# Performance work log

Hardware: AMD Instinct MI355X
Metric: run time of the kernel (lower is better)

## Reference

```python
import jax, jax.numpy as jnp
import numpy as np

B, C, D, H, W = 2, 2, 64, 256, 256
EPS = 1e-6
ALPHA = 5.0
TTEMP = 0.7


def _grids():
    gy, gx = jnp.meshgrid(jnp.arange(H, dtype=jnp.float32),
                          jnp.arange(W, dtype=jnp.float32), indexing='ij')
    return gy, gx


def _extract_targets(centerlines, gy, gx):
    # centerlines: [B,1,D,H,W] int labels {0,1,2}. For each (b,d) slice: if label i
    # occurs exactly once, target = (y,x) of that pixel, else negpair (-1,-1).
    cl = centerlines[:, 0]  # [B,D,H,W]
    out = []
    for lbl in (1, 2):
        m = (cl == lbl).astype(jnp.float32)
        cnt = m.sum(axis=(-2, -1))            # [B,D]
        ys = (m * gy).sum(axis=(-2, -1))
        xs = (m * gx).sum(axis=(-2, -1))
        t = jnp.where((cnt == 1.0)[..., None], jnp.stack([ys, xs], axis=-1), -1.0)
        out.append(t)                          # [B,D,2] float32
    return out


def _d2(gy, gx, target):
    # torch PairwiseDistance adds eps to the difference: ||x1-x2+eps||_2
    # -> [B,1,D,H,W]
    dy = gy[None, None, None] - target[:, None, :, 0, None, None] + EPS
    dx = gx[None, None, None] - target[:, None, :, 1, None, None] + EPS
    return jnp.sqrt(dy * dy + dx * dx)


def total_loss(logits, centerlines, radiuses):
    probs = jax.nn.sigmoid(logits)             # [B,2,D,H,W]
    gy, gx = _grids()
    targets = _extract_targets(centerlines, gy, gx)
    d2s = [_d2(gy, gx, t) for t in targets]
    # art masks: relu(exp(d2/r1 - 1) - 1) then filled with 1 where >0  ==  (d2 > r1);
    # the in-place fill makes it gradient-free, so treat as constant {0,1} mask.
    arts = [jax.lax.stop_gradient((d2s[k] > radiuses[k, 1]).astype(jnp.float32))
            for k in range(2)]
    arts = [arts[1], arts[0]]                  # swapped, exactly as in the source
    valid = [(t[:, :, 0] != -1.0).astype(jnp.float32) for t in targets]  # [B,D]

    # ---- CenterDistanceLoss ----
    loss_cent = jnp.float32(0.0)
    for k in range(2):
        art = arts[k]                                            # [B,1,D,H,W]
        denom = (probs * art).sum(axis=(1, 3, 4)) + EPS          # [B,D]
        y_cnt = (art * gy * probs).sum(axis=(1, 3, 4)) / denom
        x_cnt = (art * gx * probs).sum(axis=(1, 3, 4)) / denom
        cnt = jnp.stack([y_cnt, x_cnt], axis=-1)                 # [B,D,2]
        diff = cnt - targets[k] + EPS
        l2 = jnp.sqrt((diff * diff).sum(-1)) * valid[k]
        loss_cent = loss_cent + l2.mean()

    # ---- RadiusConstraintLoss ----
    loss_cnst = jnp.float32(0.0)
    for k in range(2):
        r_lu, r_ow = radiuses[k, 0], radiuses[k, 1]
        vm = valid[k][:, None, :, None, None]                    # [B,1,D,1,1]
        d2 = d2s[k]
        art = arts[k]
        lu_dout = jax.nn.relu(1.0 - jnp.exp(1.0 - d2 / r_lu)) / ALPHA * vm * art
        ow_dout = jax.nn.relu(1.0 - jnp.exp(1.0 - d2 / r_ow)) / ALPHA * vm * art
        p_lu, p_ow = probs[:, :1], probs[:, 1:]
        rc_out = ((lu_dout * p_lu).sum(axis=(1, 3, 4)) / (p_lu.sum(axis=(1, 3, 4)) + EPS)
                  + (ow_dout * p_ow).sum(axis=(1, 3, 4)) / (p_ow.sum(axis=(1, 3, 4)) + EPS))
        lu_din = jax.nn.relu(jnp.exp(1.0 - d2 / r_lu) - 1.0) * vm
        ow_din = jax.nn.relu(jnp.exp(1.0 - d2 / r_ow) - 1.0) * vm
        rc_in = ((lu_din * (1.0 - p_lu)).sum(axis=(1, 3, 4)) / (r_lu * r_lu * jnp.pi)
                 + (ow_din * (1.0 - p_ow)).sum(axis=(1, 3, 4)) / (r_ow * r_ow * jnp.pi))
        loss_cnst = loss_cnst + rc_out.mean() + rc_in.mean()

    # ---- ConsistencyLoss ----  (F.softmax default dim=1 for 5-D; BCE clamps log >= -100)
    p_orig = jax.lax.stop_gradient(jax.nn.softmax(logits[:, :, 1:-1] / TTEMP, axis=1))
    p_shift = jax.nn.softmax(logits[:, :, 0:-2] / TTEMP, axis=1)
    log_p = jnp.maximum(jnp.log(p_orig), -100.0)
    log_1mp = jnp.maximum(jnp.log(1.0 - p_orig), -100.0)
    loss_csis = -(p_shift * log_p + (1.0 - p_shift) * log_1mp).mean()

    return 0.02 * loss_cent + 1.0 * loss_cnst + 0.001 * loss_csis


def setup_inputs():
    key = jax.random.key(0)
    k1, k2, k3, k4, k5 = jax.random.split(key, 5)
    logits = jax.random.normal(k1, (B, C, D, H, W), dtype=jnp.float32)
    # place exactly one ICA(=1) and one ECA(=2) marker per (b,d) slice
    ys1 = jax.random.randint(k2, (B * D,), 0, H)
    xs1 = jax.random.randint(k3, (B * D,), 0, W)
    ys2 = jax.random.randint(k4, (B * D,), 0, H)
    xs2 = jax.random.randint(k5, (B * D,), 0, W)
    bi = jnp.repeat(jnp.arange(B), D)
    di = jnp.tile(jnp.arange(D), B)
    cl = jnp.zeros((B, 1, D, H, W), dtype=jnp.int32)
    cl = cl.at[bi, 0, di, ys1, xs1].set(1)
    cl = cl.at[bi, 0, di, ys2, xs2].set(2)
    cl = cl.at[:, :, 0].set(0)  # exercise the negpair (-1,-1) path
    radiuses = jnp.array([[4.0, 7.0], [5.0, 8.0]], dtype=jnp.float32)
    return {"logits": logits, "centerlines": cl, "radiuses": radiuses}


def reference(logits, centerlines, radiuses):
    return total_loss(logits, centerlines, radiuses)
```

## Files before the change

### kernel.cpp

```cpp
#include <hip/hip_runtime.h>
#include <math.h>

#define BB 2
#define CC 2
#define DD 64
#define HW 65536
#define NROW 128
#define EPSF 1e-6f
#define ALPHAF 5.0f
#define BPR 8
#define LOG2E 1.44269504089f
#define LN2 0.69314718056f
#define INV_T (1.0f/0.7f)
#define C_SH (INV_T*LOG2E)

struct Ws {
  int   cnt[2][NROW];
  int   ysum[2][NROW];
  int   xsum[2][NROW];
  float tgt[2][NROW][2];
  float valid[2][NROW];
  float part[NROW][BPR][17];
};

__device__ __forceinline__ void scan4(const int4& v, long long i4,
                                      Ws* __restrict__ ws) {
  if ((v.x | v.y | v.z | v.w) == 0) return;
  int vv[4] = {v.x, v.y, v.z, v.w};
#pragma unroll
  for (int e = 0; e < 4; ++e) {
    int val = vv[e];
    if (val == 1 || val == 2) {
      long long idx = i4 * 4 + e;
      int hw  = (int)(idx & (HW - 1));
      int row = (int)(idx >> 16);
      int k = val - 1;
      atomicAdd(&ws->cnt[k][row], 1);
      atomicAdd(&ws->ysum[k][row], hw >> 8);
      atomicAdd(&ws->xsum[k][row], hw & 255);
    }
  }
}

__global__ __launch_bounds__(256) void k_extract(const int* __restrict__ cl,
                                                 Ws* __restrict__ ws) {
  const long long base = (long long)blockIdx.x * 1024 + threadIdx.x;
  const int4* p = (const int4*)cl;
  int4 a = p[base];
  int4 b = p[base + 256];
  int4 c = p[base + 512];
  int4 d = p[base + 768];
  scan4(a, base, ws);
  scan4(b, base + 256, ws);
  scan4(c, base + 512, ws);
  scan4(d, base + 768, ws);
}

struct RowCtx {
  float t0y, t0x, t1y, t1x;
  float r01sq, r11sq;
  float c00, c01, c10, c11;
};

template<bool N0, bool N1>
__device__ __forceinline__ void do_row(const float4& v0, const float4& v1,
                                       const float4& w0, const float4& w1,
                                       float yf, float x0f,
                                       const RowCtx& cx, float* acc)
{
  const float a0[4] = {v0.x, v0.y, v0.z, v0.w};
  const float a1[4] = {v1.x, v1.y, v1.z, v1.w};
  const float b0[4] = {w0.x, w0.y, w0.z, w0.w};
  const float b1[4] = {w1.x, w1.y, w1.z, w1.w};
  float rp0 = 0.f, rp1 = 0.f, rcs = 0.f, rpsx = 0.f;
  float rA0 = 0.f, rA0x = 0.f, rT00 = 0.f, rT01 = 0.f;
  float rA1 = 0.f, rA1x = 0.f, rT10 = 0.f, rT11 = 0.f;
  const float dy0 = yf - cx.t0y;
  const float dy0sq = dy0 * dy0;
  const float dy1 = yf - cx.t1y;
  const float dy1sq = dy1 * dy1;
#pragma unroll
  for (int e = 0; e < 4; ++e) {
    const float le0 = a0[e], le1 = a1[e];
    const float p0 = __builtin_amdgcn_rcpf(1.f + __expf(-le0));
    const float p1 = __builtin_amdgcn_rcpf(1.f + __expf(-le1));
    rp0 += p0; rp1 += p1;
    const float psum = p0 + p1;
    const float gxf = x0f + (float)e;

    const float dshn = (le1 - le0) * C_SH;
    const float psig = __builtin_amdgcn_rcpf(1.f + exp2f(dshn));
    const float dor2 = (b0[e] - b1[e]) * C_SH;
    const float lg  = log2f(1.f + exp2f(-fabsf(dor2)));
    const float sp2 = fmaxf(dor2, 0.f) + lg;
    rcs += psig * dor2 - sp2;

    float ap0 = p0, ap1 = p1, bp0 = p0, bp1 = p1;
    float d0sq = 0.f, d1sq = 0.f;
    if (N1) {
      const float dx1 = gxf - cx.t1x;
      d1sq = fmaf(dx1, dx1, dy1sq);
      const float art0 = (d1sq > cx.r11sq) ? 1.f : 0.f;
      ap0 = art0 * p0; ap1 = art0 * p1;
      const float a0p = ap0 + ap1;
      rA0 += a0p; rA0x = fmaf(gxf, a0p, rA0x);
      if (!N0) { rT00 += ap0; rT01 += ap1; }
    }
    if (N0) {
      const float dx0 = gxf - cx.t0x;
      d0sq = fmaf(dx0, dx0, dy0sq);
      const float art1 = (d0sq > cx.r01sq) ? 1.f : 0.f;
      bp0 = art1 * p0; bp1 = art1 * p1;
      const float a1p = bp0 + bp1;
      rA1 += a1p; rA1x = fmaf(gxf, a1p, rA1x);
      if (!N1) { rT10 += bp0; rT11 += bp1; }
    }
    if (!N0 || !N1) rpsx = fmaf(gxf, psum, rpsx);

    if (N0) {
      const float dist0 = __builtin_amdgcn_sqrtf(d0sq);
      const float elu0 = exp2f(fmaf(dist0, -cx.c00, LOG2E));
      const float eow0 = exp2f(fmaf(dist0, -cx.c01, LOG2E));
      acc[8]  = fmaf(fmaxf(1.f - elu0, 0.f), ap0, acc[8]);
      acc[9]  = fmaf(fmaxf(1.f - eow0, 0.f), ap1, acc[9]);
      acc[10] = fmaf(fmaxf(elu0 - 1.f, 0.f), 1.f - p0, acc[10]);
      acc[11] = fmaf(fmaxf(eow0 - 1.f, 0.f), 1.f - p1, acc[11]);
    }
    if (N1) {
      const float dist1 = __builtin_amdgcn_sqrtf(d1sq);
      const float elu1 = exp2f(fmaf(dist1, -cx.c10, LOG2E));
      const float eow1 = exp2f(fmaf(dist1, -cx.c11, LOG2E));
      acc[12] = fmaf(fmaxf(1.f - elu1, 0.f), bp0, acc[12]);
      acc[13] = fmaf(fmaxf(1.f - eow1, 0.f), bp1, acc[13]);
      acc[14] = fmaf(fmaxf(elu1 - 1.f, 0.f), 1.f - p0, acc[14]);
      acc[15] = fmaf(fmaxf(eow1 - 1.f, 0.f), 1.f - p1, acc[15]);
    }
  }
  acc[6] += rp0; acc[7] += rp1; acc[16] += rcs;
  const float rps = rp0 + rp1;
  if (N1) { acc[0] += rA0; acc[1] = fmaf(yf, rA0, acc[1]); acc[2] += rA0x; }
  else    { acc[0] += rps; acc[1] = fmaf(yf, rps, acc[1]); acc[2] += rpsx; }
  if (N0) { acc[3] += rA1; acc[4] = fmaf(yf, rA1, acc[4]); acc[5] += rA1x; }
  else    { acc[3] += rps; acc[4] = fmaf(yf, rps, acc[4]); acc[5] += rpsx; }
  if (!N0) { acc[8]  += N1 ? rT00 : rp0; acc[9]  += N1 ? rT01 : rp1; }
  if (!N1) { acc[12] += N0 ? rT10 : rp0; acc[13] += N0 ? rT11 : rp1; }
}

#define DISPATCH_ROW(V0,V1,W0,W1,YF)                                       \
  { const bool nr0 = fabsf((YF) - cx.t0y) <= cut0;                         \
    const bool nr1 = fabsf((YF) - cx.t1y) <= cut1;                         \
    if (nr0) { if (nr1) do_row<true ,true >(V0,V1,W0,W1,YF,x0f,cx,acc);    \
               else     do_row<true ,false>(V0,V1,W0,W1,YF,x0f,cx,acc); }  \
    else     { if (nr1) do_row<false,true >(V0,V1,W0,W1,YF,x0f,cx,acc);    \
               else     do_row<false,false>(V0,V1,W0,W1,YF,x0f,cx,acc); } }

__global__ __launch_bounds__(256) void k_main(const float* __restrict__ logits,
                                              const float* __restrict__ rad,
                                              Ws* __restrict__ ws)
{
  const int row   = blockIdx.x >> 3;
  const int chunk = blockIdx.x & 7;
  const int b = row >> 6, d = row & 63;

  const int c0 = ws->cnt[0][row];
  const int c1 = ws->cnt[1][row];
  const float t0y = (c0 == 1) ? (float)ws->ysum[0][row] : -1.f;
  const float t0x = (c0 == 1) ? (float)ws->xsum[0][row] : -1.f;
  const float vld0 = (c0 == 1) ? 1.f : 0.f;
  const float t1y = (c1 == 1) ? (float)ws->ysum[1][row] : -1.f;
  const float t1x = (c1 == 1) ? (float)ws->xsum[1][row] : -1.f;
  const float vld1 = (c1 == 1) ? 1.f : 0.f;
  if (chunk == 0 && threadIdx.x == 0) {
    ws->tgt[0][row][0] = t0y; ws->tgt[0][row][1] = t0x; ws->valid[0][row] = vld0;
    ws->tgt[1][row][0] = t1y; ws->tgt[1][row][1] = t1x; ws->valid[1][row] = vld1;
  }

  const float r00 = rad[0], r01 = rad[1], r10 = rad[2], r11 = rad[3];
  RowCtx cx;
  cx.t0y = t0y - EPSF; cx.t0x = t0x - EPSF;
  cx.t1y = t1y - EPSF; cx.t1x = t1x - EPSF;
  cx.r01sq = r01 * r01; cx.r11sq = r11 * r11;
  cx.c00 = LOG2E / r00; cx.c01 = LOG2E / r01;
  cx.c10 = LOG2E / r10; cx.c11 = LOG2E / r11;
  const float cut0 = 6.f * r01, cut1 = 6.f * r11;

  const float* l0 = logits + ((long long)(b * CC + 0) * DD + d) * HW;
  const float* l1 = logits + ((long long)(b * CC + 1) * DD + d) * HW;
  const bool do_csis = (d < DD - 2);
  const long long noff = do_csis ? HW : 0;
  const float* m0 = l0 + noff;
  const float* m1 = l1 + noff;

  float acc[17];
#pragma unroll
  for (int i = 0; i < 17; ++i) acc[i] = 0.f;

  const int lane = threadIdx.x & 63;
  const int wid  = threadIdx.x >> 6;
  const float x0f = (float)(lane << 2);
  int y = chunk + (wid << 3);
  int p = (y << 8) + (lane << 2);

  float4 v0 = *(const float4*)(l0 + p);
  float4 v1 = *(const float4*)(l1 + p);
  float4 w0 = *(const float4*)(m0 + p);
  float4 w1 = *(const float4*)(m1 + p);

#pragma unroll 1
  for (int j = 0; j < 7; ++j) {
    const int pn = p + 32 * 256;
    float4 nv0 = *(const float4*)(l0 + pn);
    float4 nv1 = *(const float4*)(l1 + pn);
    float4 nw0 = *(const float4*)(m0 + pn);
    float4 nw1 = *(const float4*)(m1 + pn);
    const float yf = (float)y;
    DISPATCH_ROW(v0, v1, w0, w1, yf);
    v0 = nv0; v1 = nv1; w0 = nw0; w1 = nw1; p = pn; y += 32;
  }
  { const float yf = (float)y;
    DISPATCH_ROW(v0, v1, w0, w1, yf); }

  __shared__ float pl[4][17];
#pragma unroll
  for (int i = 0; i < 17; ++i) {
    float v = acc[i];
#pragma unroll
    for (int off = 32; off > 0; off >>= 1) v += __shfl_down(v, off, 64);
    if (lane == 0) pl[wid][i] = v;
  }
  __syncthreads();
  if (threadIdx.x < 17) {
    float s = pl[0][threadIdx.x] + pl[1][threadIdx.x] +
              pl[2][threadIdx.x] + pl[3][threadIdx.x];
    if (threadIdx.x == 16) s *= (do_csis ? LN2 : 0.f);
    ws->part[row][chunk][threadIdx.x] = s;
  }
}

__global__ void k_final(const float* __restrict__ rad,
                        const Ws* __restrict__ ws, float* __restrict__ out) {
  __shared__ float red[3][NROW];
  const int r = threadIdx.x;
  const float PI = 3.14159265358979323846f;
  float cent = 0.0f, cnst = 0.0f, csis = 0.0f;
  if (r < NROW) {
    float s[17];
#pragma unroll
    for (int i = 0; i < 17; ++i) s[i] = 0.f;
#pragma unroll
    for (int c = 0; c < BPR; ++c)
#pragma unroll
      for (int i = 0; i < 17; ++i)
        s[i] += ws->part[r][c][i];

    const float P0 = s[6], P1 = s[7];
#pragma unroll
    for (int k = 0; k < 2; ++k) {
      const float vld = ws->valid[k][r];
      const float denom = s[3 * k + 0] + EPSF;
      const float yc = s[3 * k + 1] / denom;
      const float xc = s[3 * k + 2] / denom;
      const float dy = yc - ws->tgt[k][r][0] + EPSF;
      const float dx = xc - ws->tgt[k][r][1] + EPSF;
      cent += sqrtf(dy * dy + dx * dx) * vld;
      const float r_lu = rad[2 * k], r_ow = rad[2 * k + 1];
      const int o = 8 + 4 * k;
      const float rc_out = (s[o]     / (ALPHAF * (P0 + EPSF)) +
                            s[o + 1] / (ALPHAF * (P1 + EPSF))) * vld;
      const float rc_in  = (s[o + 2] / (r_lu * r_lu * PI) +
                            s[o + 3] / (r_ow * r_ow * PI)) * vld;
      cnst += rc_out + rc_in;
    }
    csis = s[16];
  }
  red[0][r] = cent; red[1][r] = cnst; red[2][r] = csis;
  __syncthreads();
  for (int st = NROW / 2; st > 0; st >>= 1) {
    if (r < st) {
      red[0][r] += red[0][r + st];
      red[1][r] += red[1][r + st];
      red[2][r] += red[2][r + st];
    }
    __syncthreads();
  }
  if (r == 0) {
    const float inv_rows = 1.0f / (float)NROW;
    const float loss_cent = red[0][0] * inv_rows;
    const float loss_cnst = red[1][0] * inv_rows;
    const float loss_csis = -red[2][0] / (float)((long long)BB * (DD - 2) * HW);
    out[0] = 0.02f * loss_cent + loss_cnst + 0.001f * loss_csis;
  }
}

extern "C" void kernel_launch(void* const* d_in, const int* in_sizes, int n_in,
                              void* d_out, int out_size, void* d_ws, size_t ws_size,
                              hipStream_t stream) {
  const float* logits = (const float*)d_in[0];
  const int*   cl     = (const int*)d_in[1];
  const float* rad    = (const float*)d_in[2];
  Ws* ws = (Ws*)d_ws;

  hipMemsetAsync(d_ws, 0, 6 * NROW * sizeof(int), stream);
  k_extract<<<2048, 256, 0, stream>>>(cl, ws);
  k_main<<<NROW * BPR, 256, 0, stream>>>(logits, rad, ws);
  k_final<<<1, NROW, 0, stream>>>(rad, ws, (float*)d_out);
}
```

Before: 46.40 us.

## Fuse centerline target extraction into main kernel with shared-memory atomics

Removes the separate memset and extract kernel. Each row now gets two 1024-thread blocks that scan that row's full centerline slice with shared-memory atomics, then run the main loss accumulation. The two blocks per row both redo the scan, so the centerline read is doubled. Grid size drops from 1024 blocks of 256 threads to 256 blocks of 1024 threads, which changes occupancy and how load latency is hidden.

```diff
diff --git a/kernel.cpp b/kernel.cpp
--- a/kernel.cpp
+++ b/kernel.cpp
@@ -8,53 +8,16 @@
 #define NROW 128
 #define EPSF 1e-6f
 #define ALPHAF 5.0f
-#define BPR 8
 #define LOG2E 1.44269504089f
 #define LN2 0.69314718056f
 #define INV_T (1.0f/0.7f)
 #define C_SH (INV_T*LOG2E)
 
 struct Ws {
-  int   cnt[2][NROW];
-  int   ysum[2][NROW];
-  int   xsum[2][NROW];
   float tgt[2][NROW][2];
   float valid[2][NROW];
-  float part[NROW][BPR][17];
+  float part[NROW][2][17];
 };
-
-__device__ __forceinline__ void scan4(const int4& v, long long i4,
-                                      Ws* __restrict__ ws) {
-  if ((v.x | v.y | v.z | v.w) == 0) return;
-  int vv[4] = {v.x, v.y, v.z, v.w};
-#pragma unroll
-  for (int e = 0; e < 4; ++e) {
-    int val = vv[e];
-    if (val == 1 || val == 2) {
-      long long idx = i4 * 4 + e;
-      int hw  = (int)(idx & (HW - 1));
-      int row = (int)(idx >> 16);
-      int k = val - 1;
-      atomicAdd(&ws->cnt[k][row], 1);
-      atomicAdd(&ws->ysum[k][row], hw >> 8);
-      atomicAdd(&ws->xsum[k][row], hw & 255);
-    }
-  }
-}
-
-__global__ __launch_bounds__(256) void k_extract(const int* __restrict__ cl,
-                                                 Ws* __restrict__ ws) {
-  const long long base = (long long)blockIdx.x * 1024 + threadIdx.x;
-  const int4* p = (const int4*)cl;
-  int4 a = p[base];
-  int4 b = p[base + 256];
-  int4 c = p[base + 512];
-  int4 d = p[base + 768];
-  scan4(a, base, ws);
-  scan4(b, base + 256, ws);
-  scan4(c, base + 512, ws);
-  scan4(d, base + 768, ws);
-}
 
 struct RowCtx {
   float t0y, t0x, t1y, t1x;
@@ -154,25 +117,54 @@
     else     { if (nr1) do_row<false,true >(V0,V1,W0,W1,YF,x0f,cx,acc);    \
                else     do_row<false,false>(V0,V1,W0,W1,YF,x0f,cx,acc); } }
 
-__global__ __launch_bounds__(256) void k_main(const float* __restrict__ logits,
+__global__ __launch_bounds__(1024) void k_all(const float* __restrict__ logits,
+                                              const int* __restrict__ cl,
                                               const float* __restrict__ rad,
                                               Ws* __restrict__ ws)
 {
-  const int row   = blockIdx.x >> 3;
-  const int chunk = blockIdx.x & 7;
+  const int row  = blockIdx.x >> 1;
+  const int half = blockIdx.x & 1;
+  const int tid  = threadIdx.x;
+  const int lane = tid & 63;
+  const int wid  = tid >> 6;
   const int b = row >> 6, d = row & 63;
 
-  const int c0 = ws->cnt[0][row];
-  const int c1 = ws->cnt[1][row];
-  const float t0y = (c0 == 1) ? (float)ws->ysum[0][row] : -1.f;
-  const float t0x = (c0 == 1) ? (float)ws->xsum[0][row] : -1.f;
-  const float vld0 = (c0 == 1) ? 1.f : 0.f;
-  const float t1y = (c1 == 1) ? (float)ws->ysum[1][row] : -1.f;
-  const float t1x = (c1 == 1) ? (float)ws->xsum[1][row] : -1.f;
-  const float vld1 = (c1 == 1) ? 1.f : 0.f;
-  if (chunk == 0 && threadIdx.x == 0) {
-    ws->tgt[0][row][0] = t0y; ws->tgt[0][row][1] = t0x; ws->valid[0][row] = vld0;
-    ws->tgt[1][row][0] = t1y; ws->tgt[1][row][1] = t1x; ws->valid[1][row] = vld1;
+  __shared__ int sacc[6];
+  if (tid < 6) sacc[tid] = 0;
+  __syncthreads();
+  {
+    const int4* cp = (const int4*)(cl + ((long long)row << 16));
+#pragma unroll 4
+    for (int j = 0; j < 16; ++j) {
+      const int idx4 = tid + (j << 10);
+      const int4 v = cp[idx4];
+      if ((v.x | v.y | v.z | v.w) != 0) {
+        const int vv[4] = {v.x, v.y, v.z, v.w};
+#pragma unroll
+        for (int e = 0; e < 4; ++e) {
+          const int val = vv[e];
+          if (val == 1 || val == 2) {
+            const int hw = (idx4 << 2) + e;
+            const int k3 = (val - 1) * 3;
+            atomicAdd(&sacc[k3 + 0], 1);
+            atomicAdd(&sacc[k3 + 1], hw >> 8);
+            atomicAdd(&sacc[k3 + 2], hw & 255);
+          }
+        }
+      }
+    }
+  }
+  __syncthreads();
+  const int c0 = sacc[0], c1 = sacc[3];
+  const float t0y = (c0 == 1) ? (float)sacc[1] : -1.f;
+  const float t0x = (c0 == 1) ? (float)sacc[2] : -1.f;
+  const float t1y = (c1 == 1) ? (float)sacc[4] : -1.f;
+  const float t1x = (c1 == 1) ? (float)sacc[5] : -1.f;
+  if (half == 0 && tid == 0) {
+    ws->tgt[0][row][0] = t0y; ws->tgt[0][row][1] = t0x;
+    ws->valid[0][row] = (c0 == 1) ? 1.f : 0.f;
+    ws->tgt[1][row][0] = t1y; ws->tgt[1][row][1] = t1x;
+    ws->valid[1][row] = (c1 == 1) ? 1.f : 0.f;
   }
 
   const float r00 = rad[0], r01 = rad[1], r10 = rad[2], r11 = rad[3];
@@ -184,8 +176,8 @@
   cx.c10 = LOG2E / r10; cx.c11 = LOG2E / r11;
   const float cut0 = 6.f * r01, cut1 = 6.f * r11;
 
-  const float* l0 = logits + ((long long)(b * CC + 0) * DD + d) * HW;
-  const float* l1 = logits + ((long long)(b * CC + 1) * DD + d) * HW;
+  const float* l0 = logits + (((long long)(b * CC + 0) * DD + d) << 16);
+  const float* l1 = logits + (((long long)(b * CC + 1) * DD + d) << 16);
   const bool do_csis = (d < DD - 2);
   const long long noff = do_csis ? HW : 0;
   const float* m0 = l0 + noff;
@@ -195,10 +187,8 @@
 #pragma unroll
   for (int i = 0; i < 17; ++i) acc[i] = 0.f;
 
-  const int lane = threadIdx.x & 63;
-  const int wid  = threadIdx.x >> 6;
   const float x0f = (float)(lane << 2);
-  int y = chunk + (wid << 3);
+  int y = half + (wid << 1);
   int p = (y << 8) + (lane << 2);
 
   float4 v0 = *(const float4*)(l0 + p);
@@ -220,7 +210,7 @@
   { const float yf = (float)y;
     DISPATCH_ROW(v0, v1, w0, w1, yf); }
 
-  __shared__ float pl[4][17];
+  __shared__ float pl[16][17];
 #pragma unroll
   for (int i = 0; i < 17; ++i) {
     float v = acc[i];
@@ -229,11 +219,12 @@
     if (lane == 0) pl[wid][i] = v;
   }
   __syncthreads();
-  if (threadIdx.x < 17) {
-    float s = pl[0][threadIdx.x] + pl[1][threadIdx.x] +
-              pl[2][threadIdx.x] + pl[3][threadIdx.x];
-    if (threadIdx.x == 16) s *= (do_csis ? LN2 : 0.f);
-    ws->part[row][chunk][threadIdx.x] = s;
+  if (tid < 17) {
+    float s = 0.f;
+#pragma unroll
+    for (int w = 0; w < 16; ++w) s += pl[w][tid];
+    if (tid == 16) s *= (do_csis ? LN2 : 0.f);
+    ws->part[row][half][tid] = s;
   }
 }
 
@@ -246,12 +237,8 @@
   if (r < NROW) {
     float s[17];
 #pragma unroll
-    for (int i = 0; i < 17; ++i) s[i] = 0.f;
-#pragma unroll
-    for (int c = 0; c < BPR; ++c)
-#pragma unroll
-      for (int i = 0; i < 17; ++i)
-        s[i] += ws->part[r][c][i];
+    for (int i = 0; i < 17; ++i)
+      s[i] = ws->part[r][0][i] + ws->part[r][1][i];
 
     const float P0 = s[6], P1 = s[7];
 #pragma unroll
@@ -300,8 +287,6 @@
   const float* rad    = (const float*)d_in[2];
   Ws* ws = (Ws*)d_ws;
 
-  hipMemsetAsync(d_ws, 0, 6 * NROW * sizeof(int), stream);
-  k_extract<<<2048, 256, 0, stream>>>(cl, ws);
-  k_main<<<NROW * BPR, 256, 0, stream>>>(logits, rad, ws);
+  k_all<<<2 * NROW, 1024, 0, stream>>>(logits, cl, rad, ws);
   k_final<<<1, NROW, 0, stream>>>(rad, ws, (float*)d_out);
 }
```

New measurement: 44.55 us. 4.0% less time.
